# Kernel optimization log

Hardware: AMD Instinct MI355X
Metric: run time of the kernel (lower is better)

Reference implementation:

```python
import jax, jax.numpy as jnp
import numpy as np
from jax import lax

B, A, SEQ, FIN = 512, 16, 50, 6
H, H2, T, G, S = 256, 128, 60, 64, 6
GR0, GR1 = -50.0, 50.0
CELL = (GR1 - GR0) / G
NTYPES, EMB = 10, 16
NENC, NL = 5, 2

def setup_inputs() -> dict:
    key = jax.random.key(0)
    ks = jax.random.split(key, 40)
    def rn(k, shape, scale=0.05):
        return (jax.random.normal(k, shape) * scale).astype(jnp.float32)
    history = jax.random.normal(ks[0], (B, A, SEQ, FIN), dtype=jnp.float32)
    types = jax.random.randint(ks[1], (B,), 0, NTYPES)
    history = history.at[:, 0, 0, 5].set(types.astype(jnp.float32))
    d = dict(history=history)
    d['emb'] = rn(ks[2], (NTYPES, EMB))
    d['fe_W1'] = rn(ks[3], (FIN + EMB, H)); d['fe_b1'] = jnp.zeros((H,), jnp.float32)
    d['fe_W2'] = rn(ks[4], (H, H));        d['fe_b2'] = jnp.zeros((H,), jnp.float32)
    d['enc_Wih'] = rn(ks[5], (NENC, NL, H, 3 * H))
    d['enc_Whh'] = rn(ks[6], (NENC, NL, H, 3 * H))
    d['enc_bih'] = rn(ks[7], (NENC, NL, 3 * H))
    d['enc_bhh'] = rn(ks[8], (NENC, NL, 3 * H))
    d['dec_Wih0'] = rn(ks[9], (2, 3 * H)); d['dec_Whh0'] = rn(ks[10], (H, 3 * H))
    d['dec_bih0'] = rn(ks[11], (3 * H));   d['dec_bhh0'] = rn(ks[12], (3 * H))
    d['dec_Wih1'] = rn(ks[13], (H, 3 * H)); d['dec_Whh1'] = rn(ks[14], (H, 3 * H))
    d['dec_bih1'] = rn(ks[15], (3 * H));    d['dec_bhh1'] = rn(ks[16], (3 * H))
    d['hg_W1'] = rn(ks[17], (H, H));   d['hg_b1'] = jnp.zeros((H,), jnp.float32)
    d['hg_W2'] = rn(ks[18], (H, H2));  d['hg_b2'] = jnp.zeros((H2,), jnp.float32)
    d['hg_W3'] = rn(ks[19], (H2, T * 2)); d['hg_b3'] = jnp.zeros((T * 2,), jnp.float32)
    d['ce_W1'] = rn(ks[20], (H, H2));  d['ce_b1'] = jnp.zeros((H2,), jnp.float32)
    d['ce_W2'] = rn(ks[21], (H2, T));  d['ce_b2'] = jnp.zeros((T,), jnp.float32)
    d['hp_W1'] = rn(ks[22], (H, H));   d['hp_b1'] = jnp.zeros((H,), jnp.float32)
    d['hp_W2'] = rn(ks[23], (H, G * G)); d['hp_b2'] = jnp.zeros((G * G,), jnp.float32)
    return d

def _gru_cell(xt, h, Wih, Whh, bih, bhh):
    # torch GRU gate order: r, z, n
    gi = xt @ Wih + bih
    gh = h @ Whh + bhh
    Hd = h.shape[-1]
    r = jax.nn.sigmoid(gi[:, :Hd] + gh[:, :Hd])
    z = jax.nn.sigmoid(gi[:, Hd:2 * Hd] + gh[:, Hd:2 * Hd])
    n = jnp.tanh(gi[:, 2 * Hd:] + r * gh[:, 2 * Hd:])
    return (1.0 - z) * n + z * h

def _forward(history, emb, fe_W1, fe_b1, fe_W2, fe_b2,
             enc_Wih, enc_Whh, enc_bih, enc_bhh,
             dec_Wih0, dec_Whh0, dec_bih0, dec_bhh0,
             dec_Wih1, dec_Whh1, dec_bih1, dec_bhh1,
             hg_W1, hg_b1, hg_W2, hg_b2, hg_W3, hg_b3,
             ce_W1, ce_b1, ce_W2, ce_b2, hp_W1, hp_b1, hp_W2, hp_b2):
    ego = history[:, 0]                                   # [B,SEQ,6]
    etype = jnp.clip(ego[:, 0, 5].astype(jnp.int32), 0, 9)
    # type -> encoder index (vehicle,pedestrian,cyclist,bus,default)
    eidx = jnp.array([0, 1, 4, 2, 3, 4, 4, 4, 4, 4], jnp.int32)[etype]
    te = emb[etype]                                       # [B,16]
    x_in = jnp.concatenate([ego, jnp.broadcast_to(te[:, None, :], (B, SEQ, EMB))], axis=-1)
    feat = jax.nn.relu(x_in @ fe_W1 + fe_b1) @ fe_W2 + fe_b2  # [B,SEQ,H]

    # 2-layer GRU with per-example (type-gathered) weights
    x_cur = feat.transpose(1, 0, 2)                       # [SEQ,B,H]
    h_finals = []
    for l in range(NL):
        Wih = enc_Wih[eidx, l]; Whh = enc_Whh[eidx, l]    # [B,H,3H]
        bih = enc_bih[eidx, l]; bhh = enc_bhh[eidx, l]    # [B,3H]
        def step(h, xt, Wih=Wih, Whh=Whh, bih=bih, bhh=bhh):
            gi = jnp.einsum('bd,bdg->bg', xt, Wih) + bih
            gh = jnp.einsum('bh,bhg->bg', h, Whh) + bhh
            r = jax.nn.sigmoid(gi[:, :H] + gh[:, :H])
            z = jax.nn.sigmoid(gi[:, H:2 * H] + gh[:, H:2 * H])
            n = jnp.tanh(gi[:, 2 * H:] + r * gh[:, 2 * H:])
            hn = (1.0 - z) * n + z * h
            return hn, hn
        h_last, ys = lax.scan(step, jnp.zeros((B, H), feat.dtype), x_cur)
        x_cur = ys
        h_finals.append(h_last)
    enc_h0, enc_h1 = h_finals

    # decoder GRU, single timestep: x = last ego position
    x0 = ego[:, -1, :2]
    h0 = _gru_cell(x0, enc_h0, dec_Wih0, dec_Whh0, dec_bih0, dec_bhh0)
    h1 = _gru_cell(h0, enc_h1, dec_Wih1, dec_Whh1, dec_bih1, dec_bhh1)
    last_hidden = h1                                      # [B,H]

    traj = (jax.nn.relu(jax.nn.relu(last_hidden @ hg_W1 + hg_b1) @ hg_W2 + hg_b2) @ hg_W3 + hg_b3)
    traj = traj.reshape(B, T, 2)
    conf = jax.nn.relu(last_hidden @ ce_W1 + ce_b1) @ ce_W2 + ce_b2   # [B,T]

    key = jax.random.key(42)
    k_noise, k_samp = jax.random.split(key)
    noise = jax.random.normal(k_noise, (T, B, H), last_hidden.dtype)
    scale = (0.1 * jnp.arange(T, dtype=last_hidden.dtype) / T)[:, None, None]
    th = last_hidden[None] + noise * scale                # [T,B,H]
    logits = jax.nn.relu(th @ hp_W1 + hp_b1) @ hp_W2 + hp_b2  # [T,B,G*G]

    # vectorized multinomial over (samples, timesteps, batch)
    idx = jax.random.categorical(k_samp, logits, shape=(S - 1, T, B))  # int [S-1,T,B]
    x_idx = (idx % G).astype(jnp.float32)
    y_idx = (idx // G).astype(jnp.float32)
    pts = jnp.stack([GR0 + x_idx * CELL + CELL / 2,
                     GR0 + y_idx * CELL + CELL / 2], axis=-1)  # [S-1,T,B,2]
    pts = pts.transpose(2, 0, 1, 3)                       # [B,S-1,T,2]

    predictions = jnp.concatenate([traj[:, None], pts], axis=1)  # [B,S,T,2]
    decay = jnp.float32(0.9) ** jnp.arange(S, dtype=jnp.float32)
    confidences = conf.mean(axis=1)[:, None] * decay[None, :]    # [B,S]
    return predictions, confidences

def reference(history, emb, fe_W1, fe_b1, fe_W2, fe_b2,
              enc_Wih, enc_Whh, enc_bih, enc_bhh,
              dec_Wih0, dec_Whh0, dec_bih0, dec_bhh0,
              dec_Wih1, dec_Whh1, dec_bih1, dec_bhh1,
              hg_W1, hg_b1, hg_W2, hg_b2, hg_W3, hg_b3,
              ce_W1, ce_b1, ce_W2, ce_b2, hp_W1, hp_b1, hp_W2, hp_b2):
    return _forward(history, emb, fe_W1, fe_b1, fe_W2, fe_b2,
                    enc_Wih, enc_Whh, enc_bih, enc_bhh,
                    dec_Wih0, dec_Whh0, dec_bih0, dec_bhh0,
                    dec_Wih1, dec_Whh1, dec_bih1, dec_bhh1,
                    hg_W1, hg_b1, hg_W2, hg_b2, hg_W3, hg_b3,
                    ce_W1, ce_b1, ce_W2, ce_b2, hp_W1, hp_b1, hp_W2, hp_b2)
```

## Files before the change

### kernel.cpp

```cpp
#include <hip/hip_runtime.h>
#include <stdint.h>
#include <math.h>

#define JAX_PARTITIONABLE 1

#define B_ 512
#define SEQ_ 50
#define H_ 256
#define H2_ 128
#define T_ 60
#define S_ 6
#define EMB_ 16
#define NL_ 2
#define TG_ 768
#define CAT_ 4096
#define GUMBEL_N 629145600u
#define NOISE_N 7864320u

typedef float f32x2 __attribute__((ext_vector_type(2)));

#define PKFMA_LO(acc, w, h) \
  asm("v_pk_fma_f32 %0, %1, %2, %0 op_sel:[0,0,0] op_sel_hi:[1,0,1]" : "+v"(acc) : "v"(w), "v"(h))
#define PKFMA_HI(acc, w, h) \
  asm("v_pk_fma_f32 %0, %1, %2, %0 op_sel:[0,1,0] op_sel_hi:[1,1,1]" : "+v"(acc) : "v"(w), "v"(h))

__host__ __device__ inline uint32_t rotl32(uint32_t x, int r) {
#if defined(__HIP_DEVICE_COMPILE__)
  return __builtin_amdgcn_alignbit(x, x, 32 - r);
#else
  return (x << r) | (x >> (32 - r));
#endif
}

__host__ __device__ inline void tf2x32(uint32_t k0, uint32_t k1, uint32_t x0, uint32_t x1,
                                       uint32_t& o0, uint32_t& o1) {
  uint32_t ks2 = k0 ^ k1 ^ 0x1BD11BDAu;
  x0 += k0; x1 += k1;
#define TFR(r) do { x0 += x1; x1 = rotl32(x1, r); x1 ^= x0; } while (0)
  TFR(13); TFR(15); TFR(26); TFR(6);
  x0 += k1; x1 += ks2 + 1u;
  TFR(17); TFR(29); TFR(16); TFR(24);
  x0 += ks2; x1 += k0 + 2u;
  TFR(13); TFR(15); TFR(26); TFR(6);
  x0 += k0; x1 += k1 + 3u;
  TFR(17); TFR(29); TFR(16); TFR(24);
  x0 += k1; x1 += ks2 + 4u;
  TFR(13); TFR(15); TFR(26); TFR(6);
  x0 += ks2; x1 += k0 + 5u;
#undef TFR
  o0 = x0; o1 = x1;
}

__device__ inline uint32_t jax_bits(uint32_t k0, uint32_t k1, uint32_t i, uint32_t n) {
#if JAX_PARTITIONABLE
  (void)n;
  uint32_t a, b;
  tf2x32(k0, k1, 0u, i, a, b);
  return a ^ b;
#else
  uint32_t half = n >> 1;
  uint32_t lo = (i < half) ? i : (i - half);
  uint32_t a, b;
  tf2x32(k0, k1, lo, lo + half, a, b);
  return (i < half) ? a : b;
#endif
}

__device__ inline float bits_to_f01(uint32_t bits) {
  return __uint_as_float((bits >> 9) | 0x3f800000u) - 1.0f;
}

__device__ inline float erfinv_f(float x) {
  double xd = (double)x;
  float w = (float)(-log((1.0 - xd) * (1.0 + xd)));
  float p;
  if (w < 5.0f) {
    w = __fadd_rn(w, -2.5f);
    p = 2.81022636e-08f;
    p = __fadd_rn(3.43273939e-07f, __fmul_rn(p, w));
    p = __fadd_rn(-3.5233877e-06f, __fmul_rn(p, w));
    p = __fadd_rn(-4.39150654e-06f, __fmul_rn(p, w));
    p = __fadd_rn(0.00021858087f, __fmul_rn(p, w));
    p = __fadd_rn(-0.00125372503f, __fmul_rn(p, w));
    p = __fadd_rn(-0.00417768164f, __fmul_rn(p, w));
    p = __fadd_rn(0.246640727f, __fmul_rn(p, w));
    p = __fadd_rn(1.50140941f, __fmul_rn(p, w));
  } else {
    w = __fadd_rn(__fsqrt_rn(w), -3.0f);
    p = -0.000200214257f;
    p = __fadd_rn(0.000100950558f, __fmul_rn(p, w));
    p = __fadd_rn(0.00134934322f, __fmul_rn(p, w));
    p = __fadd_rn(-0.00367342844f, __fmul_rn(p, w));
    p = __fadd_rn(0.00573950773f, __fmul_rn(p, w));
    p = __fadd_rn(-0.0076224613f, __fmul_rn(p, w));
    p = __fadd_rn(0.00943887047f, __fmul_rn(p, w));
    p = __fadd_rn(1.00167406f, __fmul_rn(p, w));
    p = __fadd_rn(2.83297682f, __fmul_rn(p, w));
  }
  return __fmul_rn(p, x);
}

__device__ inline float gumbel_f32(uint32_t bits) {
  float f = bits_to_f01(bits);
  float u = fmaxf(f, 1.17549435e-38f);
  float l1 = logf(u);
  return -logf(-l1);
}

__device__ inline uint32_t orderkey(float s) {
  uint32_t sb = __float_as_uint(s);
  return (sb & 0x80000000u) ? ~sb : (sb | 0x80000000u);
}

__global__ __launch_bounds__(512) void k_init(const float* __restrict__ hist,
                                              float* __restrict__ x0buf, int* __restrict__ ip) {
  int b = threadIdx.x;
  if (b < B_) {
    float tv = hist[b * 4800 + 5];
    int et = (int)tv;
    et = et < 0 ? 0 : (et > 9 ? 9 : et);
    const int mp[10] = {0, 1, 4, 2, 3, 4, 4, 4, 4, 4};
    ip[b] = et;
    ip[512 + b] = mp[et];
    x0buf[b * 2 + 0] = hist[b * 4800 + 49 * 6 + 0];
    x0buf[b * 2 + 1] = hist[b * 4800 + 49 * 6 + 1];
  }
  __syncthreads();
  if (b == 0) {
    int cnt[5] = {0, 0, 0, 0, 0};
    for (int i = 0; i < B_; i++) cnt[ip[512 + i]]++;
    int off[6];
    off[0] = 0;
    for (int e = 0; e < 5; e++) off[e + 1] = off[e] + cnt[e];
    int pos[5];
    for (int e = 0; e < 5; e++) pos[e] = off[e];
    for (int i = 0; i < B_; i++) { int e = ip[512 + i]; ip[1024 + pos[e]++] = i; }
    int* tbl = ip + 1536;
    int nrt = 0;
    for (int e = 0; e < 5; e++) {
      int n = cnt[e];
      for (int s = 0; s < n; s += 16) {
        tbl[1 + nrt] = e;
        tbl[37 + nrt] = off[e] + s;
        tbl[73 + nrt] = (n - s) < 16 ? (n - s) : 16;
        nrt++;
      }
    }
    tbl[0] = nrt;
    int* t32 = ip + 1664;
    int n32 = 0;
    for (int e = 0; e < 5; e++) {
      int n = cnt[e];
      for (int s = 0; s < n; s += 32) {
        t32[1 + n32] = e;
        t32[21 + n32] = off[e] + s;
        t32[41 + n32] = (n - s) < 32 ? (n - s) : 32;
        n32++;
      }
    }
    t32[0] = n32;
  }
}

__global__ void k_zero(uint32_t* p, int n) {
  int i = blockIdx.x * blockDim.x + threadIdx.x;
  if (i < n) p[i] = 0u;
}

__global__ __launch_bounds__(256) void k_pack(const float* __restrict__ Wih,
                                              const float* __restrict__ Whh,
                                              float4* __restrict__ wp) {
  int i = blockIdx.x * 256 + threadIdx.x;
  if (i >= 20 * 65536) return;
  int cl = i & 31;
  int k  = (i >> 5) & 255;
  int cg = (i >> 13) & 7;
  int em = i >> 16;
  int m = em & 1;
  int el = em >> 1;
  int c = cg * 32 + cl;
  const float* W = (m ? Whh : Wih) + (size_t)el * H_ * TG_;
  float4 v;
  v.x = W[k * TG_ + c];
  v.y = W[k * TG_ + H_ + c];
  v.z = W[k * TG_ + 2 * H_ + c];
  v.w = 0.0f;
  wp[i] = v;
}

__global__ __launch_bounds__(256) void k_feat(const float* __restrict__ hist, const float* __restrict__ emb,
    const float* __restrict__ W1, const float* __restrict__ b1,
    const float* __restrict__ W2, const float* __restrict__ b2,
    const int* __restrict__ ip, float* __restrict__ featbuf) {
  __shared__ float xs[16][22];
  __shared__ float t1[16][H_];
  int row0 = blockIdx.x * 16;
  int tid = threadIdx.x;
  for (int idx = tid; idx < 16 * 22; idx += 256) {
    int r = idx / 22, c = idx % 22;
    int g = row0 + r;
    int b = g / SEQ_, s = g % SEQ_;
    xs[r][c] = (c < 6) ? hist[b * 4800 + s * 6 + c] : emb[ip[b] * EMB_ + (c - 6)];
  }
  __syncthreads();
  int j = tid;
  {
    double acc[16];
    for (int r = 0; r < 16; r++) acc[r] = 0.0;
    for (int k = 0; k < 22; k++) {
      double w = (double)W1[k * H_ + j];
      for (int r = 0; r < 16; r++) acc[r] += (double)xs[r][k] * w;
    }
    double bb = (double)b1[j];
    for (int r = 0; r < 16; r++) t1[r][j] = fmaxf((float)(acc[r] + bb), 0.0f);
  }
  __syncthreads();
  {
    double acc[16];
    for (int r = 0; r < 16; r++) acc[r] = 0.0;
    for (int k = 0; k < H_; k++) {
      double w = (double)W2[k * H_ + j];
      for (int r = 0; r < 16; r++) acc[r] += (double)t1[r][k] * w;
    }
    double bb = (double)b2[j];
    for (int r = 0; r < 16; r++) {
      float v = (float)(acc[r] + bb);
      int g = row0 + r;
      int b = g / SEQ_, s = g % SEQ_;
      featbuf[(size_t)s * (B_ * H_) + (size_t)b * H_ + j] = v;
    }
  }
}

__device__ __forceinline__ void gi_block_32(float (*xs)[H_], int* rowb,
    int rt, int cg, int tid,
    const float* __restrict__ x, float* __restrict__ gi_out,
    const float4* __restrict__ wpack, const float* __restrict__ bih_base,
    int layer, const int* __restrict__ ip) {
  const int* t32 = ip + 1664;
  const int* order = ip + 1024;
  int nrt = t32[0];
  if (rt >= nrt) return;
  int e = t32[1 + rt];
  int start = t32[21 + rt];
  int nr = t32[41 + rt];
  for (int idx = tid; idx < 32 * 64; idx += 256) {
    int r = idx >> 6, c4 = idx & 63;
    int rr = (r < nr) ? r : 0;
    int b = order[start + rr];
    if (c4 == 0) rowb[r] = b;
    *(float4*)&xs[r][c4 * 4] = *(const float4*)&x[b * H_ + c4 * 4];
  }
  __syncthreads();
  int j = tid & 31, rs = tid >> 5;
  int c = cg * 32 + j;
  int el = e * NL_ + layer;
  const float4* wp = wpack + (((size_t)(el * 2 + 0) * 8 + cg) * 256) * 32 + j;
  double a[4] = {0, 0, 0, 0}, z[4] = {0, 0, 0, 0}, n[4] = {0, 0, 0, 0};
  for (int k = 0; k < H_; k += 8) {
    float4 w[8];
#pragma unroll
    for (int kk = 0; kk < 8; kk++) w[kk] = wp[(k + kk) * 32];
    float4 xlo[4], xhi[4];
#pragma unroll
    for (int q = 0; q < 4; q++) {
      xlo[q] = *(const float4*)&xs[rs + 8 * q][k];
      xhi[q] = *(const float4*)&xs[rs + 8 * q][k + 4];
    }
#pragma unroll
    for (int kk = 0; kk < 8; kk++) {
#pragma unroll
      for (int q = 0; q < 4; q++) {
        float xv = (kk < 4) ? (&xlo[q].x)[kk] : (&xhi[q].x)[kk - 4];
        a[q] += (double)xv * (double)w[kk].x;
        z[q] += (double)xv * (double)w[kk].y;
        n[q] += (double)xv * (double)w[kk].z;
      }
    }
  }
  int cr = c, cz = H_ + c, cn = 2 * H_ + c;
  const float* bih = bih_base + (size_t)el * TG_;
  double br = (double)bih[cr], bz = (double)bih[cz], bn = (double)bih[cn];
#pragma unroll
  for (int q = 0; q < 4; q++) {
    int r = rs + 8 * q;
    if (r >= nr) continue;
    int b = rowb[r];
    gi_out[b * TG_ + cr] = (float)(a[q] + br);
    gi_out[b * TG_ + cz] = (float)(z[q] + bz);
    gi_out[b * TG_ + cn] = (float)(n[q] + bn);
  }
}

__device__ __forceinline__ void step_block_32(float (*hs)[H_], int* rowb,
    int rt, int cg, int tid,
    const float* __restrict__ gi_in, const float* __restrict__ hin,
    float* __restrict__ hout, float* __restrict__ ys,
    const float4* __restrict__ wpack, const float* __restrict__ bhh_base,
    int layer, const int* __restrict__ ip) {
  const int* t32 = ip + 1664;
  const int* order = ip + 1024;
  int nrt = t32[0];
  if (rt >= nrt) return;
  int e = t32[1 + rt];
  int start = t32[21 + rt];
  int nr = t32[41 + rt];
  for (int idx = tid; idx < 32 * 64; idx += 256) {
    int r = idx >> 6, c4 = idx & 63;
    int rr = (r < nr) ? r : 0;
    int b = order[start + rr];
    if (c4 == 0) rowb[r] = b;
    *(float4*)&hs[r][c4 * 4] = *(const float4*)&hin[b * H_ + c4 * 4];
  }
  __syncthreads();
  int j = tid & 31, rs = tid >> 5;
  int c = cg * 32 + j;
  int el = e * NL_ + layer;
  const float4* wp = wpack + (((size_t)(el * 2 + 1) * 8 + cg) * 256) * 32 + j;
  double a[4] = {0, 0, 0, 0}, z[4] = {0, 0, 0, 0}, n[4] = {0, 0, 0, 0};
  for (int k = 0; k < H_; k += 8) {
    float4 w[8];
#pragma unroll
    for (int kk = 0; kk < 8; kk++) w[kk] = wp[(k + kk) * 32];
    float4 hlo[4], hhi[4];
#pragma unroll
    for (int q = 0; q < 4; q++) {
      hlo[q] = *(const float4*)&hs[rs + 8 * q][k];
      hhi[q] = *(const float4*)&hs[rs + 8 * q][k + 4];
    }
#pragma unroll
    for (int kk = 0; kk < 8; kk++) {
#pragma unroll
      for (int q = 0; q < 4; q++) {
        float hv = (kk < 4) ? (&hlo[q].x)[kk] : (&hhi[q].x)[kk - 4];
        a[q] += (double)hv * (double)w[kk].x;
        z[q] += (double)hv * (double)w[kk].y;
        n[q] += (double)hv * (double)w[kk].z;
      }
    }
  }
  int cr = c, cz = H_ + c, cn = 2 * H_ + c;
  const float* bhh = bhh_base + (size_t)el * TG_;
  double bhr = (double)bhh[cr], bhz = (double)bhh[cz], bhn = (double)bhh[cn];
#pragma unroll
  for (int q = 0; q < 4; q++) {
    int r = rs + 8 * q;
    if (r >= nr) continue;
    int b = rowb[r];
    double gir = (double)gi_in[b * TG_ + cr];
    double giz = (double)gi_in[b * TG_ + cz];
    double gin = (double)gi_in[b * TG_ + cn];
    double ghr = a[q] + bhr;
    double ghz = z[q] + bhz;
    double ghn = n[q] + bhn;
    double rr = 1.0 / (1.0 + exp(-(gir + ghr)));
    double zz = 1.0 / (1.0 + exp(-(giz + ghz)));
    double nn = tanh(gin + rr * ghn);
    double hv = (double)hs[r][c];
    float hnew = (float)((1.0 - zz) * nn + zz * hv);
    hout[b * H_ + c] = hnew;
    if (ys) ys[b * H_ + c] = hnew;
  }
}

__global__ __launch_bounds__(256) void k_pipe32(int d,
    const float* __restrict__ feat, float* __restrict__ ys0,
    float* __restrict__ gi0, float* __restrict__ gi1,
    float* __restrict__ h0A, float* __restrict__ h0B,
    float* __restrict__ h1A, float* __restrict__ h1B,
    const float4* __restrict__ wpack,
    const float* __restrict__ bih, const float* __restrict__ bhh,
    const int* __restrict__ ip) {
  __shared__ float sb[32][H_];
  __shared__ int rowb[32];
  int g = blockIdx.x;
  int grp = g / 160, bx = g % 160;
  int rt = bx >> 3, cg = bx & 7;
  int tid = threadIdx.x;
  if (grp == 0) {
    int t = d;
    if (t < SEQ_)
      gi_block_32(sb, rowb, rt, cg, tid, feat + (size_t)t * 131072,
                  gi0 + (size_t)(t & 1) * 393216, wpack, bih, 0, ip);
  } else if (grp == 1) {
    int t = d - 1;
    if (t >= 0 && t < SEQ_) {
      const float* hin = (t & 1) ? h0B : h0A;
      float* hout = (t & 1) ? h0A : h0B;
      step_block_32(sb, rowb, rt, cg, tid, gi0 + (size_t)(t & 1) * 393216,
                    hin, hout, ys0 + (size_t)t * 131072, wpack, bhh, 0, ip);
    }
  } else if (grp == 2) {
    int t = d - 2;
    if (t >= 0 && t < SEQ_)
      gi_block_32(sb, rowb, rt, cg, tid, ys0 + (size_t)t * 131072,
                  gi1 + (size_t)(t & 1) * 393216, wpack, bih, 1, ip);
  } else {
    int t = d - 3;
    if (t >= 0 && t < SEQ_) {
      const float* hin = (t & 1) ? h1B : h1A;
      float* hout = (t & 1) ? h1A : h1B;
      step_block_32(sb, rowb, rt, cg, tid, gi1 + (size_t)(t & 1) * 393216,
                    hin, hout, nullptr, wpack, bhh, 1, ip);
    }
  }
}

__device__ __forceinline__ void gi_block_u(float (*xs)[H_], int* rowb,
    int rt, int cg, int tid,
    const float* __restrict__ x, float* __restrict__ gi_out,
    const float* __restrict__ Wih_base, const float* __restrict__ bih_base,
    int layer, const int* __restrict__ ip) {
  const int* tbl = ip + 1536;
  const int* order = ip + 1024;
  int nrt = tbl[0];
  if (rt >= nrt) return;
  int e = tbl[1 + rt];
  int start = tbl[37 + rt];
  int nr = tbl[73 + rt];
  for (int idx = tid; idx < 16 * H_; idx += 256) {
    int r = idx >> 8, k = idx & 255;
    int rr = (r < nr) ? r : 0;
    int b = order[start + rr];
    if (k == 0) rowb[r] = b;
    xs[r][k] = x[b * H_ + k];
  }
  __syncthreads();
  size_t woff = (size_t)(e * NL_ + layer);
  const float* Wih = Wih_base + woff * (size_t)H_ * TG_;
  const float* bih = bih_base + woff * TG_;
  int j = tid & 31, rs = tid >> 5;
  int c = cg * 32 + j;
  int cr = c, cz = H_ + c, cn = 2 * H_ + c;
  double ar0 = 0, ar1 = 0, az0 = 0, az1 = 0, an0 = 0, an1 = 0;
  for (int k = 0; k < H_; k++) {
    float wr = Wih[k * TG_ + cr], wz = Wih[k * TG_ + cz], wn = Wih[k * TG_ + cn];
    float x0 = xs[rs][k], x1 = xs[rs + 8][k];
    ar0 += (double)x0 * wr; ar1 += (double)x1 * wr;
    az0 += (double)x0 * wz; az1 += (double)x1 * wz;
    an0 += (double)x0 * wn; an1 += (double)x1 * wn;
  }
  double br = (double)bih[cr], bz = (double)bih[cz], bn = (double)bih[cn];
  for (int p = 0; p < 2; p++) {
    int r = rs + 8 * p;
    if (r >= nr) continue;
    int b = rowb[r];
    gi_out[b * TG_ + cr] = (float)((p ? ar1 : ar0) + br);
    gi_out[b * TG_ + cz] = (float)((p ? az1 : az0) + bz);
    gi_out[b * TG_ + cn] = (float)((p ? an1 : an0) + bn);
  }
}

__device__ __forceinline__ void step_block_u(float (*hs)[H_], int* rowb,
    int rt, int cg, int tid,
    const float* __restrict__ gi_in, const float* __restrict__ hin,
    float* __restrict__ hout, float* __restrict__ ys,
    const float* __restrict__ Whh_base, const float* __restrict__ bhh_base,
    int layer, const int* __restrict__ ip) {
  const int* tbl = ip + 1536;
  const int* order = ip + 1024;
  int nrt = tbl[0];
  if (rt >= nrt) return;
  int e = tbl[1 + rt];
  int start = tbl[37 + rt];
  int nr = tbl[73 + rt];
  for (int idx = tid; idx < 16 * H_; idx += 256) {
    int r = idx >> 8, k = idx & 255;
    int rr = (r < nr) ? r : 0;
    int b = order[start + rr];
    if (k == 0) rowb[r] = b;
    hs[r][k] = hin[b * H_ + k];
  }
  __syncthreads();
  size_t woff = (size_t)(e * NL_ + layer);
  const float* Whh = Whh_base + woff * (size_t)H_ * TG_;
  const float* bhh = bhh_base + woff * TG_;
  int j = tid & 31, rs = tid >> 5;
  int c = cg * 32 + j;
  int cr = c, cz = H_ + c, cn = 2 * H_ + c;
  double gr0 = 0, gr1 = 0, gz0 = 0, gz1 = 0, gn0 = 0, gn1 = 0;
  for (int k = 0; k < H_; k++) {
    float wr = Whh[k * TG_ + cr], wz = Whh[k * TG_ + cz], wn = Whh[k * TG_ + cn];
    float h0 = hs[rs][k], h1 = hs[rs + 8][k];
    gr0 += (double)h0 * wr; gr1 += (double)h1 * wr;
    gz0 += (double)h0 * wz; gz1 += (double)h1 * wz;
    gn0 += (double)h0 * wn; gn1 += (double)h1 * wn;
  }
  double bhr = (double)bhh[cr], bhz = (double)bhh[cz], bhn = (double)bhh[cn];
  for (int p = 0; p < 2; p++) {
    int r = rs + 8 * p;
    if (r >= nr) continue;
    int b = rowb[r];
    double gir = (double)gi_in[b * TG_ + cr];
    double giz = (double)gi_in[b * TG_ + cz];
    double gin = (double)gi_in[b * TG_ + cn];
    double ghr = (p ? gr1 : gr0) + bhr;
    double ghz = (p ? gz1 : gz0) + bhz;
    double ghn = (p ? gn1 : gn0) + bhn;
    double rr = 1.0 / (1.0 + exp(-(gir + ghr)));
    double zz = 1.0 / (1.0 + exp(-(giz + ghz)));
    double nn = tanh(gin + rr * ghn);
    double hv = (double)hs[r][c];
    float hnew = (float)((1.0 - zz) * nn + zz * hv);
    hout[b * H_ + c] = hnew;
    if (ys) ys[b * H_ + c] = hnew;
  }
}

__global__ __launch_bounds__(256) void k_pipeu(int d,
    const float* __restrict__ feat, float* __restrict__ ys0,
    float* __restrict__ gi0, float* __restrict__ gi1,
    float* __restrict__ h0A, float* __restrict__ h0B,
    float* __restrict__ h1A, float* __restrict__ h1B,
    const float* __restrict__ Wih, const float* __restrict__ Whh,
    const float* __restrict__ bih, const float* __restrict__ bhh,
    const int* __restrict__ ip) {
  __shared__ float sb[16][H_];
  __shared__ int rowb[16];
  int g = blockIdx.x;
  int grp = g / 288, bx = g % 288;
  int rt = bx >> 3, cg = bx & 7;
  int tid = threadIdx.x;
  if (grp == 0) {
    int t = d; if (t >= SEQ_) return;
    gi_block_u(sb, rowb, rt, cg, tid, feat + (size_t)t * 131072,
               gi0 + (size_t)(t & 1) * 393216, Wih, bih, 0, ip);
  } else if (grp == 1) {
    int t = d - 1; if (t < 0 || t >= SEQ_) return;
    const float* hin = (t & 1) ? h0B : h0A;
    float* hout = (t & 1) ? h0A : h0B;
    step_block_u(sb, rowb, rt, cg, tid, gi0 + (size_t)(t & 1) * 393216,
                 hin, hout, ys0 + (size_t)t * 131072, Whh, bhh, 0, ip);
  } else if (grp == 2) {
    int t = d - 2; if (t < 0 || t >= SEQ_) return;
    gi_block_u(sb, rowb, rt, cg, tid, ys0 + (size_t)t * 131072,
               gi1 + (size_t)(t & 1) * 393216, Wih, bih, 1, ip);
  } else {
    int t = d - 3; if (t < 0 || t >= SEQ_) return;
    const float* hin = (t & 1) ? h1B : h1A;
    float* hout = (t & 1) ? h1A : h1B;
    step_block_u(sb, rowb, rt, cg, tid, gi1 + (size_t)(t & 1) * 393216,
                 hin, hout, nullptr, Whh, bhh, 1, ip);
  }
}

template <int D1>
__global__ __launch_bounds__(256) void k_gru(
    const float* __restrict__ x, const float* __restrict__ hin,
    float* __restrict__ hout,
    const float* __restrict__ Wih, const float* __restrict__ Whh,
    const float* __restrict__ bih, const float* __restrict__ bhh) {
  __shared__ float xs[16][(D1 == 2) ? 2 : H_];
  __shared__ float hs[16][H_];
  int bx = blockIdx.x, by = blockIdx.y;
  int start = bx * 16;
  int tid = threadIdx.x;
  for (int idx = tid; idx < 16 * H_; idx += 256) {
    int r = idx >> 8, k = idx & 255;
    int b = start + r;
    hs[r][k] = hin[b * H_ + k];
    if (D1 == H_) xs[r][k] = x[b * H_ + k];
    else if (k < D1) xs[r][k] = x[b * D1 + k];
  }
  __syncthreads();
  int j = tid & 31, rs = tid >> 5;
  int hc = by * 32 + j;
  int cr = hc, cz = H_ + hc, cn = 2 * H_ + hc;
  double ra0 = 0, ra1 = 0, za0 = 0, za1 = 0, ni0 = 0, ni1 = 0, nh0 = 0, nh1 = 0;
  for (int k = 0; k < H_; k++) {
    float wrh = Whh[k * TG_ + cr], wzh = Whh[k * TG_ + cz], wnh = Whh[k * TG_ + cn];
    float h0v = hs[rs][k], h1v = hs[rs + 8][k];
    ra0 += (double)h0v * wrh; ra1 += (double)h1v * wrh;
    za0 += (double)h0v * wzh; za1 += (double)h1v * wzh;
    nh0 += (double)h0v * wnh; nh1 += (double)h1v * wnh;
    if (D1 == H_) {
      float wri = Wih[k * TG_ + cr], wzi = Wih[k * TG_ + cz], wni = Wih[k * TG_ + cn];
      float x0v = xs[rs][k], x1v = xs[rs + 8][k];
      ra0 += (double)x0v * wri; ra1 += (double)x1v * wri;
      za0 += (double)x0v * wzi; za1 += (double)x1v * wzi;
      ni0 += (double)x0v * wni; ni1 += (double)x1v * wni;
    }
  }
  if (D1 != H_) {
    for (int k = 0; k < D1; k++) {
      float wri = Wih[k * TG_ + cr], wzi = Wih[k * TG_ + cz], wni = Wih[k * TG_ + cn];
      float x0v = xs[rs][k], x1v = xs[rs + 8][k];
      ra0 += (double)x0v * wri; ra1 += (double)x1v * wri;
      za0 += (double)x0v * wzi; za1 += (double)x1v * wzi;
      ni0 += (double)x0v * wni; ni1 += (double)x1v * wni;
    }
  }
  double br_i = (double)bih[cr], bz_i = (double)bih[cz], bn_i = (double)bih[cn];
  double br_h = (double)bhh[cr], bz_h = (double)bhh[cz], bn_h = (double)bhh[cn];
  for (int p = 0; p < 2; p++) {
    int r = rs + 8 * p;
    double ra = p ? ra1 : ra0, za = p ? za1 : za0, ni = p ? ni1 : ni0, nh = p ? nh1 : nh0;
    double rr = 1.0 / (1.0 + exp(-(ra + br_i + br_h)));
    double zz = 1.0 / (1.0 + exp(-(za + bz_i + bz_h)));
    double nn = tanh((ni + bn_i) + rr * (nh + bn_h));
    double hv = (double)hs[r][hc];
    float hnew = (float)((1.0 - zz) * nn + zz * hv);
    hout[(start + r) * H_ + hc] = hnew;
  }
}

__global__ __launch_bounds__(256) void k_heads(const float* __restrict__ lh,
    const float* __restrict__ hgW1, const float* __restrict__ hgb1,
    const float* __restrict__ hgW2, const float* __restrict__ hgb2,
    const float* __restrict__ hgW3, const float* __restrict__ hgb3,
    const float* __restrict__ ceW1, const float* __restrict__ ceb1,
    const float* __restrict__ ceW2, const float* __restrict__ ceb2,
    float* __restrict__ out) {
  __shared__ float hsm[16][H_];
  __shared__ float t1[16][H_];
  __shared__ float t2[16][H2_];
  __shared__ float c2s[16][T_];
  int row0 = blockIdx.x * 16;
  int tid = threadIdx.x;
  for (int idx = tid; idx < 16 * H_; idx += 256) {
    int r = idx >> 8, k = idx & 255;
    hsm[r][k] = lh[(size_t)(row0 + r) * H_ + k];
  }
  __syncthreads();
  {
    int j = tid;
    for (int r = 0; r < 16; r++) {
      double a = 0;
      for (int k = 0; k < H_; k++) a += (double)hsm[r][k] * (double)hgW1[k * H_ + j];
      t1[r][j] = fmaxf((float)(a + (double)hgb1[j]), 0.0f);
    }
  }
  __syncthreads();
  if (tid < H2_) {
    int j = tid;
    for (int r = 0; r < 16; r++) {
      double a = 0;
      for (int k = 0; k < H_; k++) a += (double)t1[r][k] * (double)hgW2[k * H2_ + j];
      t2[r][j] = fmaxf((float)(a + (double)hgb2[j]), 0.0f);
    }
  }
  __syncthreads();
  if (tid < 2 * T_) {
    int j = tid;
    for (int r = 0; r < 16; r++) {
      double a = 0;
      for (int k = 0; k < H2_; k++) a += (double)t2[r][k] * (double)hgW3[k * (2 * T_) + j];
      float v = (float)(a + (double)hgb3[j]);
      int b = row0 + r;
      int t = j >> 1, c = j & 1;
      out[(((size_t)b * S_ + 0) * T_ + t) * 2 + c] = v;
    }
  }
  __syncthreads();
  if (tid < H2_) {
    int j = tid;
    for (int r = 0; r < 16; r++) {
      double a = 0;
      for (int k = 0; k < H_; k++) a += (double)hsm[r][k] * (double)ceW1[k * H2_ + j];
      t2[r][j] = fmaxf((float)(a + (double)ceb1[j]), 0.0f);
    }
  }
  __syncthreads();
  if (tid < T_) {
    int j = tid;
    for (int r = 0; r < 16; r++) {
      double a = 0;
      for (int k = 0; k < H2_; k++) a += (double)t2[r][k] * (double)ceW2[k * T_ + j];
      c2s[r][j] = (float)(a + (double)ceb2[j]);
    }
  }
  __syncthreads();
  if (tid < 16) {
    int r = tid;
    int b = row0 + r;
    double s = 0;
    for (int j = 0; j < T_; j++) s += (double)c2s[r][j];
    float m = (float)(s / 60.0);
    for (int sd = 0; sd < S_; sd++) {
      float d = (float)pow((double)0.9f, (double)sd);
      out[368640 + b * S_ + sd] = __fmul_rn(m, d);
    }
  }
}

__global__ __launch_bounds__(256) void k_hp1(const float* __restrict__ lh,
    const float* __restrict__ W1, const float* __restrict__ b1,
    float* __restrict__ h1buf, uint32_t nk0, uint32_t nk1) {
  __shared__ float th[16][H_];
  int row0 = blockIdx.x * 16;
  int tid = threadIdx.x;
  const float SQRT2F = 1.4142135623730951f;
  const float LO = -0x1.fffffep-1f;
  for (int idx = tid; idx < 16 * H_; idx += 256) {
    int r = idx >> 8, k = idx & 255;
    int g = row0 + r;
    int t = g / B_, b = g % B_;
    uint32_t i = ((uint32_t)t * B_ + (uint32_t)b) * H_ + (uint32_t)k;
    uint32_t bits = jax_bits(nk0, nk1, i, NOISE_N);
    float f = bits_to_f01(bits);
    float u = fmaxf(LO, __fadd_rn(__fmul_rn(f, 2.0f), LO));
    float nz = __fmul_rn(SQRT2F, erfinv_f(u));
    float sc = __fdiv_rn(__fmul_rn(0.1f, (float)t), 60.0f);
    th[r][k] = __fadd_rn(lh[(size_t)b * H_ + k], __fmul_rn(nz, sc));
  }
  __syncthreads();
  int j = tid;
  double acc[16];
  for (int r = 0; r < 16; r++) acc[r] = 0.0;
  for (int k = 0; k < H_; k++) {
    double w = (double)W1[k * H_ + j];
    for (int r = 0; r < 16; r++) acc[r] += (double)th[r][k] * w;
  }
  double bb = (double)b1[j];
  for (int r = 0; r < 16; r++)
    h1buf[(size_t)(row0 + r) * H_ + j] = fmaxf((float)(acc[r] + bb), 0.0f);
}

__global__ __launch_bounds__(256) void k_hp2(const float* __restrict__ h1buf,
    const float* __restrict__ W2, const float* __restrict__ b2,
    unsigned long long* __restrict__ samples, uint32_t sk0, uint32_t sk1) {
  __shared__ float h1[16][H_];
  int row0 = blockIdx.x * 16;
  int cat0 = blockIdx.y * 256;
  int tid = threadIdx.x;
  for (int idx = tid; idx < 16 * H_ / 4; idx += 256) {
    int r = idx >> 6, k4 = (idx & 63) << 2;
    *(float4*)&h1[r][k4] = *(const float4*)&h1buf[(size_t)(row0 + r) * H_ + k4];
  }
  __syncthreads();
  int wave = tid >> 6;
  int lane = tid & 63;
  int catA = cat0 + 4 * lane;
  int rbase = 4 * wave;

  f32x2 acc[4][2];
#pragma unroll
  for (int r = 0; r < 4; r++) { acc[r][0] = (f32x2)0.0f; acc[r][1] = (f32x2)0.0f; }
  const float* w2p = W2 + catA;
  for (int k = 0; k < H_; k += 4) {
    float4 hv[4];
    hv[0] = *(const float4*)&h1[rbase + 0][k];
    hv[1] = *(const float4*)&h1[rbase + 1][k];
    hv[2] = *(const float4*)&h1[rbase + 2][k];
    hv[3] = *(const float4*)&h1[rbase + 3][k];
    float4 wv[4];
#pragma unroll
    for (int kk = 0; kk < 4; kk++) wv[kk] = *(const float4*)&w2p[(size_t)(k + kk) * CAT_];
#pragma unroll
    for (int kk = 0; kk < 4; kk++) {
      f32x2 wlo; wlo.x = wv[kk].x; wlo.y = wv[kk].y;
      f32x2 whi; whi.x = wv[kk].z; whi.y = wv[kk].w;
#pragma unroll
      for (int r = 0; r < 4; r++) {
        f32x2 hp;
        if (kk & 2) { hp.x = (&hv[r].x)[2]; hp.y = (&hv[r].x)[3]; }
        else        { hp.x = (&hv[r].x)[0]; hp.y = (&hv[r].x)[1]; }
        if (kk & 1) { PKFMA_HI(acc[r][0], wlo, hp); PKFMA_HI(acc[r][1], whi, hp); }
        else        { PKFMA_LO(acc[r][0], wlo, hp); PKFMA_LO(acc[r][1], whi, hp); }
      }
    }
  }
  float lg[4][4];
  float4 b4 = *(const float4*)&b2[catA];
#pragma unroll
  for (int r = 0; r < 4; r++) {
    lg[r][0] = __fadd_rn(acc[r][0].x, b4.x);
    lg[r][1] = __fadd_rn(acc[r][0].y, b4.y);
    lg[r][2] = __fadd_rn(acc[r][1].x, b4.z);
    lg[r][3] = __fadd_rn(acc[r][1].y, b4.w);
  }

  int t = row0 / B_;
  int bbase = row0 % B_;
#pragma unroll
  for (int s = 0; s < S_ - 1; s++) {
#pragma unroll
    for (int q = 0; q < 4; q++) {
      int brow = bbase + rbase + q;
      uint32_t ibase = (((uint32_t)s * T_ + (uint32_t)t) * B_ + (uint32_t)brow) * CAT_ + (uint32_t)catA;
      float sc0 = __fadd_rn(gumbel_f32(jax_bits(sk0, sk1, ibase + 0u, GUMBEL_N)), lg[q][0]);
      float sc1 = __fadd_rn(gumbel_f32(jax_bits(sk0, sk1, ibase + 1u, GUMBEL_N)), lg[q][1]);
      float sc2 = __fadd_rn(gumbel_f32(jax_bits(sk0, sk1, ibase + 2u, GUMBEL_N)), lg[q][2]);
      float sc3 = __fadd_rn(gumbel_f32(jax_bits(sk0, sk1, ibase + 3u, GUMBEL_N)), lg[q][3]);
      float bs = sc0; int bc = catA;
      if (sc1 > bs) { bs = sc1; bc = catA + 1; }
      if (sc2 > bs) { bs = sc2; bc = catA + 2; }
      if (sc3 > bs) { bs = sc3; bc = catA + 3; }
      float mv = bs;
      for (int off = 1; off < 64; off <<= 1)
        mv = fmaxf(mv, __shfl_xor(mv, off, 64));
      unsigned long long mask = __ballot(bs == mv);
      int src = __ffsll(mask) - 1;
      int wcat = __shfl(bc, src, 64);
      if (lane == 0) {
        unsigned long long p =
            (((unsigned long long)orderkey(mv)) << 32) | (unsigned long long)(~(uint32_t)wcat);
        atomicMax(&samples[((size_t)s * T_ + t) * B_ + brow], p);
      }
    }
  }
}

__global__ void k_emit(const unsigned long long* __restrict__ samples, float* __restrict__ out) {
  int gid = blockIdx.x * blockDim.x + threadIdx.x;
  if (gid >= (S_ - 1) * T_ * B_) return;
  int b = gid % B_;
  int t = (gid / B_) % T_;
  int s = gid / (B_ * T_);
  unsigned long long v = samples[gid];
  uint32_t cat = ~(uint32_t)(v & 0xFFFFFFFFu);
  float xi = (float)(cat & 63u);
  float yi = (float)(cat >> 6);
  float px = -50.0f + xi * 1.5625f + 0.78125f;
  float py = -50.0f + yi * 1.5625f + 0.78125f;
  size_t o = (((size_t)b * S_ + (size_t)(s + 1)) * T_ + t) * 2;
  out[o] = px;
  out[o + 1] = py;
}

extern "C" void kernel_launch(void* const* d_in, const int* in_sizes, int n_in,
                              void* d_out, int out_size, void* d_ws, size_t ws_size,
                              hipStream_t stream) {
  (void)in_sizes; (void)n_in; (void)out_size;
  const float* hist   = (const float*)d_in[0];
  const float* emb    = (const float*)d_in[1];
  const float* feW1   = (const float*)d_in[2];
  const float* feb1   = (const float*)d_in[3];
  const float* feW2   = (const float*)d_in[4];
  const float* feb2   = (const float*)d_in[5];
  const float* encWih = (const float*)d_in[6];
  const float* encWhh = (const float*)d_in[7];
  const float* encbih = (const float*)d_in[8];
  const float* encbhh = (const float*)d_in[9];
  const float* dWih0  = (const float*)d_in[10];
  const float* dWhh0  = (const float*)d_in[11];
  const float* dbih0  = (const float*)d_in[12];
  const float* dbhh0  = (const float*)d_in[13];
  const float* dWih1  = (const float*)d_in[14];
  const float* dWhh1  = (const float*)d_in[15];
  const float* dbih1  = (const float*)d_in[16];
  const float* dbhh1  = (const float*)d_in[17];
  const float* hgW1   = (const float*)d_in[18];
  const float* hgb1   = (const float*)d_in[19];
  const float* hgW2   = (const float*)d_in[20];
  const float* hgb2   = (const float*)d_in[21];
  const float* hgW3   = (const float*)d_in[22];
  const float* hgb3   = (const float*)d_in[23];
  const float* ceW1   = (const float*)d_in[24];
  const float* ceb1   = (const float*)d_in[25];
  const float* ceW2   = (const float*)d_in[26];
  const float* ceb2   = (const float*)d_in[27];
  const float* hpW1   = (const float*)d_in[28];
  const float* hpb1   = (const float*)d_in[29];
  const float* hpW2   = (const float*)d_in[30];
  const float* hpb2   = (const float*)d_in[31];
  float* out = (float*)d_out;
  float* ws = (float*)d_ws;

  float* feat  = ws;
  float* ys0   = ws + 6553600;
  float* gi0   = ws + 13107200;
  float* gi1   = ws + 13893632;
  float* h0A   = ws + 14680064;
  float* h0B   = h0A + 131072;
  float* h1A   = h0B + 131072;
  float* h1B   = h1A + 131072;
  float* dech0 = h1B + 131072;
  float* lh    = dech0 + 131072;
  float* x0buf = lh + 131072;
  int*   ip    = (int*)(x0buf + 1024);
  unsigned long long* samples =
      (unsigned long long*)(((uintptr_t)(ip + 2048) + 255) & ~(uintptr_t)255);
  float* h1hp  = ws;

  size_t samples_end = (size_t)((char*)(samples + 307200) - (char*)ws);
  size_t wpack_off = (samples_end + 255) & ~(size_t)255;
  float4* wpack = (float4*)((char*)ws + wpack_off);
  bool packed = (wpack_off + (size_t)20 * 65536 * 16) <= ws_size;

  uint32_t kn0, kn1, ks0, ks1;
#if JAX_PARTITIONABLE
  tf2x32(0u, 42u, 0u, 0u, kn0, kn1);
  tf2x32(0u, 42u, 0u, 1u, ks0, ks1);
#else
  { uint32_t a0, a1, b0, b1;
    tf2x32(0u, 42u, 0u, 2u, a0, a1);
    tf2x32(0u, 42u, 1u, 3u, b0, b1);
    kn0 = a0; kn1 = b0; ks0 = a1; ks1 = b1; }
#endif

  k_init<<<dim3(1), dim3(512), 0, stream>>>(hist, x0buf, ip);
  k_zero<<<dim3((524288 + 255) / 256), dim3(256), 0, stream>>>((uint32_t*)h0A, 524288);
  k_zero<<<dim3((307200 + 255) / 256), dim3(256), 0, stream>>>((uint32_t*)samples, 307200);
  if (packed)
    k_pack<<<dim3(5120), dim3(256), 0, stream>>>(encWih, encWhh, wpack);
  k_feat<<<dim3(1600), dim3(256), 0, stream>>>(hist, emb, feW1, feb1, feW2, feb2, ip, feat);

  if (packed) {
    for (int d = 0; d < SEQ_ + 3; d++)
      k_pipe32<<<dim3(640), dim3(256), 0, stream>>>(d,
          feat, ys0, gi0, gi1, h0A, h0B, h1A, h1B,
          wpack, encbih, encbhh, ip);
  } else {
    for (int d = 0; d < SEQ_ + 3; d++)
      k_pipeu<<<dim3(1152), dim3(256), 0, stream>>>(d,
          feat, ys0, gi0, gi1, h0A, h0B, h1A, h1B,
          encWih, encWhh, encbih, encbhh, ip);
  }

  k_gru<2><<<dim3(32, 8), dim3(256), 0, stream>>>(
      x0buf, h0A, dech0, dWih0, dWhh0, dbih0, dbhh0);
  k_gru<H_><<<dim3(32, 8), dim3(256), 0, stream>>>(
      dech0, h1A, lh, dWih1, dWhh1, dbih1, dbhh1);

  k_heads<<<dim3(32), dim3(256), 0, stream>>>(lh, hgW1, hgb1, hgW2, hgb2, hgW3, hgb3,
                                              ceW1, ceb1, ceW2, ceb2, out);
  k_hp1<<<dim3(1920), dim3(256), 0, stream>>>(lh, hpW1, hpb1, h1hp, kn0, kn1);
  k_hp2<<<dim3(1920, 16), dim3(256), 0, stream>>>(h1hp, hpW2, hpb2, samples, ks0, ks1);
  k_emit<<<dim3(600), dim3(256), 0, stream>>>(samples, out);
}
```

Measured before the change: 5.500 ms.

## Use exponential-race sampling and pre-widen encoder weights to double

```diff
diff --git a/kernel.cpp b/kernel.cpp
--- a/kernel.cpp
+++ b/kernel.cpp
@@ -100,13 +100,6 @@
   return __fmul_rn(p, x);
 }
 
-__device__ inline float gumbel_f32(uint32_t bits) {
-  float f = bits_to_f01(bits);
-  float u = fmaxf(f, 1.17549435e-38f);
-  float l1 = logf(u);
-  return -logf(-l1);
-}
-
 __device__ inline uint32_t orderkey(float s) {
   uint32_t sb = __float_as_uint(s);
   return (sb & 0x80000000u) ? ~sb : (sb | 0x80000000u);
@@ -162,14 +155,14 @@
   }
 }
 
-__global__ void k_zero(uint32_t* p, int n) {
+__global__ void k_fill(uint32_t* p, int n, uint32_t v) {
   int i = blockIdx.x * blockDim.x + threadIdx.x;
-  if (i < n) p[i] = 0u;
+  if (i < n) p[i] = v;
 }
 
 __global__ __launch_bounds__(256) void k_pack(const float* __restrict__ Wih,
                                               const float* __restrict__ Whh,
-                                              float4* __restrict__ wp) {
+                                              double4* __restrict__ wp) {
   int i = blockIdx.x * 256 + threadIdx.x;
   if (i >= 20 * 65536) return;
   int cl = i & 31;
@@ -180,11 +173,11 @@
   int el = em >> 1;
   int c = cg * 32 + cl;
   const float* W = (m ? Whh : Wih) + (size_t)el * H_ * TG_;
-  float4 v;
-  v.x = W[k * TG_ + c];
-  v.y = W[k * TG_ + H_ + c];
-  v.z = W[k * TG_ + 2 * H_ + c];
-  v.w = 0.0f;
+  double4 v;
+  v.x = (double)W[k * TG_ + c];
+  v.y = (double)W[k * TG_ + H_ + c];
+  v.z = (double)W[k * TG_ + 2 * H_ + c];
+  v.w = 0.0;
   wp[i] = v;
 }
 
@@ -235,7 +228,7 @@
 __device__ __forceinline__ void gi_block_32(float (*xs)[H_], int* rowb,
     int rt, int cg, int tid,
     const float* __restrict__ x, float* __restrict__ gi_out,
-    const float4* __restrict__ wpack, const float* __restrict__ bih_base,
+    const double4* __restrict__ wpack, const float* __restrict__ bih_base,
     int layer, const int* __restrict__ ip) {
   const int* t32 = ip + 1664;
   const int* order = ip + 1024;
@@ -255,26 +248,23 @@
   int j = tid & 31, rs = tid >> 5;
   int c = cg * 32 + j;
   int el = e * NL_ + layer;
-  const float4* wp = wpack + (((size_t)(el * 2 + 0) * 8 + cg) * 256) * 32 + j;
+  const double4* wp = wpack + (((size_t)(el * 2 + 0) * 8 + cg) * 256) * 32 + j;
   double a[4] = {0, 0, 0, 0}, z[4] = {0, 0, 0, 0}, n[4] = {0, 0, 0, 0};
-  for (int k = 0; k < H_; k += 8) {
-    float4 w[8];
-#pragma unroll
-    for (int kk = 0; kk < 8; kk++) w[kk] = wp[(k + kk) * 32];
-    float4 xlo[4], xhi[4];
-#pragma unroll
-    for (int q = 0; q < 4; q++) {
-      xlo[q] = *(const float4*)&xs[rs + 8 * q][k];
-      xhi[q] = *(const float4*)&xs[rs + 8 * q][k + 4];
-    }
-#pragma unroll
-    for (int kk = 0; kk < 8; kk++) {
+  for (int k = 0; k < H_; k += 4) {
+    double4 w[4];
+#pragma unroll
+    for (int kk = 0; kk < 4; kk++) w[kk] = wp[(k + kk) * 32];
+    float4 xv4[4];
+#pragma unroll
+    for (int q = 0; q < 4; q++) xv4[q] = *(const float4*)&xs[rs + 8 * q][k];
+#pragma unroll
+    for (int kk = 0; kk < 4; kk++) {
 #pragma unroll
       for (int q = 0; q < 4; q++) {
-        float xv = (kk < 4) ? (&xlo[q].x)[kk] : (&xhi[q].x)[kk - 4];
-        a[q] += (double)xv * (double)w[kk].x;
-        z[q] += (double)xv * (double)w[kk].y;
-        n[q] += (double)xv * (double)w[kk].z;
+        double xv = (double)(&xv4[q].x)[kk];
+        a[q] += xv * w[kk].x;
+        z[q] += xv * w[kk].y;
+        n[q] += xv * w[kk].z;
       }
     }
   }
@@ -296,7 +286,7 @@
     int rt, int cg, int tid,
     const float* __restrict__ gi_in, const float* __restrict__ hin,
     float* __restrict__ hout, float* __restrict__ ys,
-    const float4* __restrict__ wpack, const float* __restrict__ bhh_base,
+    const double4* __restrict__ wpack, const float* __restrict__ bhh_base,
     int layer, const int* __restrict__ ip) {
   const int* t32 = ip + 1664;
   const int* order = ip + 1024;
@@ -316,26 +306,23 @@
   int j = tid & 31, rs = tid >> 5;
   int c = cg * 32 + j;
   int el = e * NL_ + layer;
-  const float4* wp = wpack + (((size_t)(el * 2 + 1) * 8 + cg) * 256) * 32 + j;
+  const double4* wp = wpack + (((size_t)(el * 2 + 1) * 8 + cg) * 256) * 32 + j;
   double a[4] = {0, 0, 0, 0}, z[4] = {0, 0, 0, 0}, n[4] = {0, 0, 0, 0};
-  for (int k = 0; k < H_; k += 8) {
-    float4 w[8];
-#pragma unroll
-    for (int kk = 0; kk < 8; kk++) w[kk] = wp[(k + kk) * 32];
-    float4 hlo[4], hhi[4];
-#pragma unroll
-    for (int q = 0; q < 4; q++) {
-      hlo[q] = *(const float4*)&hs[rs + 8 * q][k];
-      hhi[q] = *(const float4*)&hs[rs + 8 * q][k + 4];
-    }
-#pragma unroll
-    for (int kk = 0; kk < 8; kk++) {
+  for (int k = 0; k < H_; k += 4) {
+    double4 w[4];
+#pragma unroll
+    for (int kk = 0; kk < 4; kk++) w[kk] = wp[(k + kk) * 32];
+    float4 hv4[4];
+#pragma unroll
+    for (int q = 0; q < 4; q++) hv4[q] = *(const float4*)&hs[rs + 8 * q][k];
+#pragma unroll
+    for (int kk = 0; kk < 4; kk++) {
 #pragma unroll
       for (int q = 0; q < 4; q++) {
-        float hv = (kk < 4) ? (&hlo[q].x)[kk] : (&hhi[q].x)[kk - 4];
-        a[q] += (double)hv * (double)w[kk].x;
-        z[q] += (double)hv * (double)w[kk].y;
-        n[q] += (double)hv * (double)w[kk].z;
+        double hv = (double)(&hv4[q].x)[kk];
+        a[q] += hv * w[kk].x;
+        z[q] += hv * w[kk].y;
+        n[q] += hv * w[kk].z;
       }
     }
   }
@@ -368,7 +355,7 @@
     float* __restrict__ gi0, float* __restrict__ gi1,
     float* __restrict__ h0A, float* __restrict__ h0B,
     float* __restrict__ h1A, float* __restrict__ h1B,
-    const float4* __restrict__ wpack,
+    const double4* __restrict__ wpack,
     const float* __restrict__ bih, const float* __restrict__ bhh,
     const int* __restrict__ ip) {
   __shared__ float sb[32][H_];
@@ -760,16 +747,17 @@
       }
     }
   }
-  float lg[4][4];
+  float el[4][4];
   float4 b4 = *(const float4*)&b2[catA];
 #pragma unroll
   for (int r = 0; r < 4; r++) {
-    lg[r][0] = __fadd_rn(acc[r][0].x, b4.x);
-    lg[r][1] = __fadd_rn(acc[r][0].y, b4.y);
-    lg[r][2] = __fadd_rn(acc[r][1].x, b4.z);
-    lg[r][3] = __fadd_rn(acc[r][1].y, b4.w);
-  }
-
+    el[r][0] = expf(-__fadd_rn(acc[r][0].x, b4.x));
+    el[r][1] = expf(-__fadd_rn(acc[r][0].y, b4.y));
+    el[r][2] = expf(-__fadd_rn(acc[r][1].x, b4.z));
+    el[r][3] = expf(-__fadd_rn(acc[r][1].y, b4.w));
+  }
+
+  const float FMIN = 1.17549435e-38f;
   int t = row0 / B_;
   int bbase = row0 % B_;
 #pragma unroll
@@ -778,24 +766,31 @@
     for (int q = 0; q < 4; q++) {
       int brow = bbase + rbase + q;
       uint32_t ibase = (((uint32_t)s * T_ + (uint32_t)t) * B_ + (uint32_t)brow) * CAT_ + (uint32_t)catA;
-      float sc0 = __fadd_rn(gumbel_f32(jax_bits(sk0, sk1, ibase + 0u, GUMBEL_N)), lg[q][0]);
-      float sc1 = __fadd_rn(gumbel_f32(jax_bits(sk0, sk1, ibase + 1u, GUMBEL_N)), lg[q][1]);
-      float sc2 = __fadd_rn(gumbel_f32(jax_bits(sk0, sk1, ibase + 2u, GUMBEL_N)), lg[q][2]);
-      float sc3 = __fadd_rn(gumbel_f32(jax_bits(sk0, sk1, ibase + 3u, GUMBEL_N)), lg[q][3]);
-      float bs = sc0; int bc = catA;
-      if (sc1 > bs) { bs = sc1; bc = catA + 1; }
-      if (sc2 > bs) { bs = sc2; bc = catA + 2; }
-      if (sc3 > bs) { bs = sc3; bc = catA + 3; }
+      float w0, w1, w2, w3;
+      {
+        float u0 = fmaxf(bits_to_f01(jax_bits(sk0, sk1, ibase + 0u, GUMBEL_N)), FMIN);
+        float u1 = fmaxf(bits_to_f01(jax_bits(sk0, sk1, ibase + 1u, GUMBEL_N)), FMIN);
+        float u2 = fmaxf(bits_to_f01(jax_bits(sk0, sk1, ibase + 2u, GUMBEL_N)), FMIN);
+        float u3 = fmaxf(bits_to_f01(jax_bits(sk0, sk1, ibase + 3u, GUMBEL_N)), FMIN);
+        w0 = __fmul_rn(-logf(u0), el[q][0]);
+        w1 = __fmul_rn(-logf(u1), el[q][1]);
+        w2 = __fmul_rn(-logf(u2), el[q][2]);
+        w3 = __fmul_rn(-logf(u3), el[q][3]);
+      }
+      float bs = w0; int bc = catA;
+      if (w1 < bs) { bs = w1; bc = catA + 1; }
+      if (w2 < bs) { bs = w2; bc = catA + 2; }
+      if (w3 < bs) { bs = w3; bc = catA + 3; }
       float mv = bs;
       for (int off = 1; off < 64; off <<= 1)
-        mv = fmaxf(mv, __shfl_xor(mv, off, 64));
+        mv = fminf(mv, __shfl_xor(mv, off, 64));
       unsigned long long mask = __ballot(bs == mv);
       int src = __ffsll(mask) - 1;
       int wcat = __shfl(bc, src, 64);
       if (lane == 0) {
         unsigned long long p =
-            (((unsigned long long)orderkey(mv)) << 32) | (unsigned long long)(~(uint32_t)wcat);
-        atomicMax(&samples[((size_t)s * T_ + t) * B_ + brow], p);
+            (((unsigned long long)orderkey(mv)) << 32) | (unsigned long long)(uint32_t)wcat;
+        atomicMin(&samples[((size_t)s * T_ + t) * B_ + brow], p);
       }
     }
   }
@@ -808,7 +803,7 @@
   int t = (gid / B_) % T_;
   int s = gid / (B_ * T_);
   unsigned long long v = samples[gid];
-  uint32_t cat = ~(uint32_t)(v & 0xFFFFFFFFu);
+  uint32_t cat = (uint32_t)(v & 0xFFFFFFFFu);
   float xi = (float)(cat & 63u);
   float yi = (float)(cat >> 6);
   float px = -50.0f + xi * 1.5625f + 0.78125f;
@@ -875,8 +870,8 @@
 
   size_t samples_end = (size_t)((char*)(samples + 307200) - (char*)ws);
   size_t wpack_off = (samples_end + 255) & ~(size_t)255;
-  float4* wpack = (float4*)((char*)ws + wpack_off);
-  bool packed = (wpack_off + (size_t)20 * 65536 * 16) <= ws_size;
+  double4* wpack = (double4*)((char*)ws + wpack_off);
+  bool packed = (wpack_off + (size_t)20 * 65536 * 32) <= ws_size;
 
   uint32_t kn0, kn1, ks0, ks1;
 #if JAX_PARTITIONABLE
@@ -890,8 +885,8 @@
 #endif
 
   k_init<<<dim3(1), dim3(512), 0, stream>>>(hist, x0buf, ip);
-  k_zero<<<dim3((524288 + 255) / 256), dim3(256), 0, stream>>>((uint32_t*)h0A, 524288);
-  k_zero<<<dim3((307200 + 255) / 256), dim3(256), 0, stream>>>((uint32_t*)samples, 307200);
+  k_fill<<<dim3((524288 + 255) / 256), dim3(256), 0, stream>>>((uint32_t*)h0A, 524288, 0u);
+  k_fill<<<dim3((307200 + 255) / 256), dim3(256), 0, stream>>>((uint32_t*)samples, 307200, 0xFFFFFFFFu);
   if (packed)
     k_pack<<<dim3(5120), dim3(256), 0, stream>>>(encWih, encWhh, wpack);
   k_feat<<<dim3(1600), dim3(256), 0, stream>>>(hist, emb, feW1, feb1, feW2, feb2, ip, feat);
```

New measurement: 6.190 ms. +12.6%, slower.
